# Kernel tuning notes

Measured on AMD Instinct MI355X. Metric: run time of the kernel, lower is better.

Reference implementation:

```python
import jax, jax.numpy as jnp
import numpy as np

HIDDEN = 256


def setup_inputs() -> dict:
    key = jax.random.key(0)
    k1, k2 = jax.random.split(key)
    B, N, K, Q = 32, 20, 5, 15
    support = jax.random.normal(k1, (B * N * K, HIDDEN), dtype=jnp.float32)
    query = jax.random.normal(k2, (B * N * Q, HIDDEN), dtype=jnp.float32)
    return {"support": support, "query": query, "N": N, "K": K, "Q": Q}


def reference(support, query, N, K, Q):
    # support: [B*N*K, H] -> [B, N, K, H]; query: [B*N*Q, H] -> [B, N*Q, H]
    H = support.shape[-1]
    S = support.reshape(-1, N, K, H)
    Qr = query.reshape(-1, N * Q, H)
    proto = jnp.mean(S, axis=2)  # [B, N, H]
    # squared Euclidean distance: S.unsqueeze(1) - Q.unsqueeze(2)
    # diff: [B, N*Q, N, H] -> sum over H -> [B, N*Q, N]
    diff = proto[:, None, :, :] - Qr[:, :, None, :]
    logits = -jnp.sum(diff * diff, axis=3)
    return logits
```

## Files before the change

### kernel.cpp

```cpp
#include <hip/hip_runtime.h>


#define HDIM 256
#define NN   20
#define KK   5
#define NQ   300
#define TQ   12
#define PAD  260

__global__ __launch_bounds__(256) void proto_dist_kernel(
    const float* __restrict__ support,
    const float* __restrict__ query,
    float* __restrict__ out)
{
    __shared__ float proto[NN * PAD];

    const int blocksPerB = NQ / TQ;
    const int b   = blockIdx.x / blocksPerB;
    const int qb  = (blockIdx.x % blocksPerB) * TQ;
    const int tid = threadIdx.x;

    {
        const int h4 = (tid & 63) * 4;
        const int g  = tid >> 6;
        for (int n = g; n < NN; n += 4) {
            const float* sp = support + ((size_t)(b * NN + n) * KK) * HDIM + h4;
            float4 acc = make_float4(0.f, 0.f, 0.f, 0.f);
            #pragma unroll
            for (int k = 0; k < KK; ++k) {
                float4 v = *reinterpret_cast<const float4*>(sp + (size_t)k * HDIM);
                acc.x += v.x; acc.y += v.y; acc.z += v.z; acc.w += v.w;
            }
            const float inv = 1.0f / KK;
            float4 r = make_float4(acc.x * inv, acc.y * inv, acc.z * inv, acc.w * inv);
            *reinterpret_cast<float4*>(&proto[n * PAD + h4]) = r;
        }
    }
    __syncthreads();

    if (tid < TQ * NN) {
        const int q = qb + tid / NN;
        const int n = tid % NN;
        const float* qp = query + (size_t)(b * NQ + q) * HDIM;
        const float* pp = &proto[n * PAD];
        float acc = 0.f;
        #pragma unroll 8
        for (int h = 0; h < HDIM; h += 4) {
            float4 qv = *reinterpret_cast<const float4*>(qp + h);
            float4 pv = *reinterpret_cast<const float4*>(pp + h);
            float dx = pv.x - qv.x;
            float dy = pv.y - qv.y;
            float dz = pv.z - qv.z;
            float dw = pv.w - qv.w;
            acc += dx * dx + dy * dy + dz * dz + dw * dw;
        }
        out[(size_t)(b * NQ + q) * NN + n] = -acc;
    }
}

extern "C" void kernel_launch(void* const* d_in, const int* in_sizes, int n_in,
                              void* d_out, int out_size, void* d_ws, size_t ws_size,
                              hipStream_t stream) {
    const float* support = (const float*)d_in[0];
    const float* query   = (const float*)d_in[1];
    float* out = (float*)d_out;

    const int B = in_sizes[0] / (NN * KK * HDIM);
    dim3 grid(B * (NQ / TQ));
    proto_dist_kernel<<<grid, dim3(256), 0, stream>>>(support, query, out);
}
```

Measured before the change: 20.20 us.

## Split prototype mean into separate kernel and register-block queries per thread

Prototype means are now computed once per episode by a dedicated kernel into workspace, instead of being recomputed by every query block. The distance kernel uses 64-thread blocks where each thread handles one prototype against four queries, reusing the prototype load across them and keeping independent per-component accumulators. This removes the redundant support reads and the shared-memory barrier. In exchange it adds a second kernel launch and a global round trip for the prototypes, and it leaves 4 of 64 lanes idle with small blocks.

```diff
diff --git a/kernel.cpp b/kernel.cpp
--- a/kernel.cpp
+++ b/kernel.cpp
@@ -5,56 +5,86 @@
 #define NN   20
 #define KK   5
 #define NQ   300
-#define TQ   12
-#define PAD  260
 
-__global__ __launch_bounds__(256) void proto_dist_kernel(
+__global__ __launch_bounds__(256) void proto_mean_kernel(
     const float* __restrict__ support,
+    float* __restrict__ proto)
+{
+    const int wid  = blockIdx.x * 4 + (threadIdx.x >> 6);
+    const int lane = threadIdx.x & 63;
+    const float* sp = support + (size_t)wid * (KK * HDIM) + lane * 4;
+    float4 acc = make_float4(0.f, 0.f, 0.f, 0.f);
+    #pragma unroll
+    for (int k = 0; k < KK; ++k) {
+        float4 v = *reinterpret_cast<const float4*>(sp + (size_t)k * HDIM);
+        acc.x += v.x; acc.y += v.y; acc.z += v.z; acc.w += v.w;
+    }
+    const float inv = 1.0f / KK;
+    float4 r = make_float4(acc.x * inv, acc.y * inv, acc.z * inv, acc.w * inv);
+    *reinterpret_cast<float4*>(proto + (size_t)wid * HDIM + lane * 4) = r;
+}
+
+__global__ __launch_bounds__(64) void proto_dist_kernel(
+    const float* __restrict__ proto,
     const float* __restrict__ query,
     float* __restrict__ out)
 {
-    __shared__ float proto[NN * PAD];
+    const int b     = blockIdx.x / 25;
+    const int qbase = (blockIdx.x % 25) * 12;
+    const int lane  = threadIdx.x;
 
-    const int blocksPerB = NQ / TQ;
-    const int b   = blockIdx.x / blocksPerB;
-    const int qb  = (blockIdx.x % blocksPerB) * TQ;
-    const int tid = threadIdx.x;
+    if (lane < 60) {
+        const int n  = lane % 20;
+        const int qg = lane / 20;
 
-    {
-        const int h4 = (tid & 63) * 4;
-        const int g  = tid >> 6;
-        for (int n = g; n < NN; n += 4) {
-            const float* sp = support + ((size_t)(b * NN + n) * KK) * HDIM + h4;
-            float4 acc = make_float4(0.f, 0.f, 0.f, 0.f);
-            #pragma unroll
-            for (int k = 0; k < KK; ++k) {
-                float4 v = *reinterpret_cast<const float4*>(sp + (size_t)k * HDIM);
-                acc.x += v.x; acc.y += v.y; acc.z += v.z; acc.w += v.w;
-            }
-            const float inv = 1.0f / KK;
-            float4 r = make_float4(acc.x * inv, acc.y * inv, acc.z * inv, acc.w * inv);
-            *reinterpret_cast<float4*>(&proto[n * PAD + h4]) = r;
-        }
-    }
-    __syncthreads();
+        const float* pp = proto + (size_t)(b * NN + n) * HDIM;
+        const float* qp = query + (size_t)(b * NQ + qbase + qg * 4) * HDIM;
 
-    if (tid < TQ * NN) {
-        const int q = qb + tid / NN;
-        const int n = tid % NN;
-        const float* qp = query + (size_t)(b * NQ + q) * HDIM;
-        const float* pp = &proto[n * PAD];
-        float acc = 0.f;
+        float4 a0 = make_float4(0.f, 0.f, 0.f, 0.f);
+        float4 a1 = make_float4(0.f, 0.f, 0.f, 0.f);
+        float4 a2 = make_float4(0.f, 0.f, 0.f, 0.f);
+        float4 a3 = make_float4(0.f, 0.f, 0.f, 0.f);
+
         #pragma unroll 8
         for (int h = 0; h < HDIM; h += 4) {
-            float4 qv = *reinterpret_cast<const float4*>(qp + h);
             float4 pv = *reinterpret_cast<const float4*>(pp + h);
-            float dx = pv.x - qv.x;
-            float dy = pv.y - qv.y;
-            float dz = pv.z - qv.z;
-            float dw = pv.w - qv.w;
-            acc += dx * dx + dy * dy + dz * dz + dw * dw;
+            float4 q0 = *reinterpret_cast<const float4*>(qp + h);
+            float4 q1 = *reinterpret_cast<const float4*>(qp + HDIM + h);
+            float4 q2 = *reinterpret_cast<const float4*>(qp + 2 * HDIM + h);
+            float4 q3 = *reinterpret_cast<const float4*>(qp + 3 * HDIM + h);
+
+            float d;
+            d = pv.x - q0.x; a0.x += d * d;
+            d = pv.y - q0.y; a0.y += d * d;
+            d = pv.z - q0.z; a0.z += d * d;
+            d = pv.w - q0.w; a0.w += d * d;
+
+            d = pv.x - q1.x; a1.x += d * d;
+            d = pv.y - q1.y; a1.y += d * d;
+            d = pv.z - q1.z; a1.z += d * d;
+            d = pv.w - q1.w; a1.w += d * d;
+
+            d = pv.x - q2.x; a2.x += d * d;
+            d = pv.y - q2.y; a2.y += d * d;
+            d = pv.z - q2.z; a2.z += d * d;
+            d = pv.w - q2.w; a2.w += d * d;
+
+            d = pv.x - q3.x; a3.x += d * d;
+            d = pv.y - q3.y; a3.y += d * d;
+            d = pv.z - q3.z; a3.z += d * d;
+            d = pv.w - q3.w; a3.w += d * d;
         }
-        out[(size_t)(b * NQ + q) * NN + n] = -acc;
+
+        float s0 = a0.x + a0.y + a0.z + a0.w;
+        float s1 = a1.x + a1.y + a1.z + a1.w;
+        float s2 = a2.x + a2.y + a2.z + a2.w;
+        float s3 = a3.x + a3.y + a3.z + a3.w;
+
+        float* op = out + ((size_t)(b * NQ + qbase + qg * 4)) * NN + n;
+        op[0 * NN] = -s0;
+        op[1 * NN] = -s1;
+        op[2 * NN] = -s2;
+        op[3 * NN] = -s3;
     }
 }
 
@@ -63,9 +93,11 @@
                               hipStream_t stream) {
     const float* support = (const float*)d_in[0];
     const float* query   = (const float*)d_in[1];
-    float* out = (float*)d_out;
+    float* out   = (float*)d_out;
+    float* proto = (float*)d_ws;
 
     const int B = in_sizes[0] / (NN * KK * HDIM);
-    dim3 grid(B * (NQ / TQ));
-    proto_dist_kernel<<<grid, dim3(256), 0, stream>>>(support, query, out);
+
+    proto_mean_kernel<<<dim3(B * NN / 4), dim3(256), 0, stream>>>(support, proto);
+    proto_dist_kernel<<<dim3(B * (NQ / 12)), dim3(64), 0, stream>>>(proto, query, out);
 }
```

Measured after the change: 28.41 us. +40.7%, slower.

## Use norm expansion for distances and compute two queries per thread

Applied to the files above, without the earlier changes.

Rewrites the squared distance as 2·p·q − |p|² − |q|², with the prototype and query norms computed once per block through wave shuffle reductions and kept in shared memory. Each thread now accumulates dot products for two queries against one prototype, so every prototype load from shared memory is reused. The query tile grows from 12 to 20, which gives fewer blocks per batch and less repeated prototype-mean work. The expanded form can lose some floating-point precision through cancellation, and the larger tile lowers the total block count.

```diff
diff --git a/kernel.cpp b/kernel.cpp
--- a/kernel.cpp
+++ b/kernel.cpp
@@ -5,8 +5,11 @@
 #define NN   20
 #define KK   5
 #define NQ   300
-#define TQ   12
+#define TQ   20
 #define PAD  260
+#define NBLK_PER_B (NQ / TQ)
+
+typedef float f32x4 __attribute__((ext_vector_type(4)));
 
 __global__ __launch_bounds__(256) void proto_dist_kernel(
     const float* __restrict__ support,
@@ -14,47 +17,71 @@
     float* __restrict__ out)
 {
     __shared__ float proto[NN * PAD];
+    __shared__ float normP[NN];
+    __shared__ float normQ[TQ];
 
-    const int blocksPerB = NQ / TQ;
-    const int b   = blockIdx.x / blocksPerB;
-    const int qb  = (blockIdx.x % blocksPerB) * TQ;
-    const int tid = threadIdx.x;
+    const int b     = blockIdx.x / NBLK_PER_B;
+    const int qbase = (blockIdx.x % NBLK_PER_B) * TQ;
+    const int tid   = threadIdx.x;
+    const int wave  = tid >> 6;
+    const int lane  = tid & 63;
+    const int h4    = lane * 4;
 
-    {
-        const int h4 = (tid & 63) * 4;
-        const int g  = tid >> 6;
-        for (int n = g; n < NN; n += 4) {
-            const float* sp = support + ((size_t)(b * NN + n) * KK) * HDIM + h4;
-            float4 acc = make_float4(0.f, 0.f, 0.f, 0.f);
-            #pragma unroll
-            for (int k = 0; k < KK; ++k) {
-                float4 v = *reinterpret_cast<const float4*>(sp + (size_t)k * HDIM);
-                acc.x += v.x; acc.y += v.y; acc.z += v.z; acc.w += v.w;
-            }
-            const float inv = 1.0f / KK;
-            float4 r = make_float4(acc.x * inv, acc.y * inv, acc.z * inv, acc.w * inv);
-            *reinterpret_cast<float4*>(&proto[n * PAD + h4]) = r;
+    #pragma unroll
+    for (int i = 0; i < 5; ++i) {
+        const int n = wave * 5 + i;
+        const float* sp = support + ((size_t)(b * NN + n) * KK) * HDIM + h4;
+        f32x4 acc = {0.f, 0.f, 0.f, 0.f};
+        #pragma unroll
+        for (int k = 0; k < KK; ++k) {
+            f32x4 v = *reinterpret_cast<const f32x4*>(sp + k * HDIM);
+            acc += v;
         }
+        acc *= 0.2f;
+        *reinterpret_cast<f32x4*>(&proto[n * PAD + h4]) = acc;
+        float s = acc.x * acc.x + acc.y * acc.y + acc.z * acc.z + acc.w * acc.w;
+        #pragma unroll
+        for (int m = 32; m >= 1; m >>= 1) s += __shfl_xor(s, m, 64);
+        if (lane == 0) normP[n] = s;
+    }
+
+    #pragma unroll
+    for (int i = 0; i < 5; ++i) {
+        const int r = wave * 5 + i;
+        f32x4 v = *reinterpret_cast<const f32x4*>(
+            query + (size_t)(b * NQ + qbase + r) * HDIM + h4);
+        float s = v.x * v.x + v.y * v.y + v.z * v.z + v.w * v.w;
+        #pragma unroll
+        for (int m = 32; m >= 1; m >>= 1) s += __shfl_xor(s, m, 64);
+        if (lane == 0) normQ[r] = s;
     }
     __syncthreads();
 
-    if (tid < TQ * NN) {
-        const int q = qb + tid / NN;
-        const int n = tid % NN;
-        const float* qp = query + (size_t)(b * NQ + q) * HDIM;
-        const float* pp = &proto[n * PAD];
-        float acc = 0.f;
+    if (tid < 200) {
+        const int qg = tid / NN;
+        const int n  = tid % NN;
+        const int q0 = qg * 2;
+        const float* qp0 = query + (size_t)(b * NQ + qbase + q0) * HDIM;
+        const float* qp1 = qp0 + HDIM;
+        const float* pp  = &proto[n * PAD];
+
+        f32x4 a0 = {0.f, 0.f, 0.f, 0.f};
+        f32x4 a1 = {0.f, 0.f, 0.f, 0.f};
         #pragma unroll 8
         for (int h = 0; h < HDIM; h += 4) {
-            float4 qv = *reinterpret_cast<const float4*>(qp + h);
-            float4 pv = *reinterpret_cast<const float4*>(pp + h);
-            float dx = pv.x - qv.x;
-            float dy = pv.y - qv.y;
-            float dz = pv.z - qv.z;
-            float dw = pv.w - qv.w;
-            acc += dx * dx + dy * dy + dz * dz + dw * dw;
+            f32x4 pv = *reinterpret_cast<const f32x4*>(pp + h);
+            f32x4 v0 = *reinterpret_cast<const f32x4*>(qp0 + h);
+            f32x4 v1 = *reinterpret_cast<const f32x4*>(qp1 + h);
+            a0 += pv * v0;
+            a1 += pv * v1;
         }
-        out[(size_t)(b * NQ + q) * NN + n] = -acc;
+        const float s0 = a0.x + a0.y + a0.z + a0.w;
+        const float s1 = a1.x + a1.y + a1.z + a1.w;
+        const float pn = normP[n];
+
+        float* op = out + ((size_t)(b * NQ + qbase + q0)) * NN + n;
+        op[0]  = 2.f * s0 - pn - normQ[q0];
+        op[NN] = 2.f * s1 - pn - normQ[q0 + 1];
     }
 }
 
@@ -66,6 +93,5 @@
     float* out = (float*)d_out;
 
     const int B = in_sizes[0] / (NN * KK * HDIM);
-    dim3 grid(B * (NQ / TQ));
-    proto_dist_kernel<<<grid, dim3(256), 0, stream>>>(support, query, out);
+    proto_dist_kernel<<<dim3(B * NBLK_PER_B), dim3(256), 0, stream>>>(support, query, out);
 }
```

Result: no change. 20.40 us (+1.0%).
